# Optimization experiments

Hardware: AMD Instinct MI355X
Metric: run time of the kernel (lower is better)

## Reference

```python
import jax, jax.numpy as jnp
import numpy as np

N_NODES = 50000
N_EDGES = 800000
NFEAT = 512
NHID = 64
NHEADS = 8
NCLASS = 40
ALPHA = 0.2  # LeakyReLU slope
EPS = 1e-16  # guards isolated-node division


def setup_inputs() -> dict:
    key = jax.random.key(0)
    k = jax.random.split(key, 6)
    x = jax.random.normal(k[0], (N_NODES, NFEAT), dtype=jnp.float32)
    W_heads = jax.random.normal(k[1], (NHEADS, NFEAT, NHID), dtype=jnp.float32) * 0.05
    a_heads = jax.random.normal(k[2], (NHEADS, 2 * NHID), dtype=jnp.float32) * 0.05
    W_out = jax.random.normal(k[3], (NHEADS * NHID, NCLASS), dtype=jnp.float32) * 0.05
    a_out = jax.random.normal(k[4], (2 * NCLASS,), dtype=jnp.float32) * 0.05
    edge_index = jax.random.randint(k[5], (2, N_EDGES), 0, N_NODES, dtype=jnp.int32)
    return {"x": x, "W_heads": W_heads, "a_heads": a_heads,
            "W_out": W_out, "a_out": a_out, "edge_index": edge_index}


def _gat_layer(x, W, a, row, col, concat):
    # pyGAT sparse layer: h = xW; e_ij = exp(-LeakyReLU(a^T [h_i || h_j]));
    # out_i = sum_j e_ij h_j / sum_j e_ij   (aggregate into row, gather from col)
    D = W.shape[1]
    h = x @ W                                            # [N, D]
    score = h[row] @ a[:D] + h[col] @ a[D:]              # [E]
    e = jnp.exp(-jax.nn.leaky_relu(score, ALPHA))        # [E]
    num = jax.ops.segment_sum(e[:, None] * h[col], row, num_segments=x.shape[0])  # [N, D]
    den = jax.ops.segment_sum(e, row, num_segments=x.shape[0])                    # [N]
    out = num / (den[:, None] + EPS)
    return jax.nn.elu(out) if concat else out


def reference(x, W_heads, a_heads, W_out, a_out, edge_index):
    # dropout layers are identity in eval mode (training=False)
    row, col = edge_index[0], edge_index[1]
    heads = jax.vmap(lambda W, a: _gat_layer(x, W, a, row, col, True))(W_heads, a_heads)
    # [H, N, D] -> [N, H*D] (concat along feature dim, head-major like torch.cat)
    hcat = jnp.transpose(heads, (1, 0, 2)).reshape(x.shape[0], -1)
    return _gat_layer(hcat, W_out, a_out, row, col, False)  # [N, NCLASS]
```

## Files before the change

### kernel.cpp

```cpp
#include <hip/hip_runtime.h>
#include <hip/hip_bf16.h>

#define N_NODES 50000
#define N_EDGES 800000
#define NFEAT   512
#define NHID    64
#define NHEADS  8
#define NCLASS  40
#define HD      (NHEADS*NHID)
#define ALPHA   0.2f
#define EPS_F   1e-16f
#define NCHUNK  ((N_NODES + 255)/256)

typedef __attribute__((ext_vector_type(8))) short short8;
typedef __attribute__((ext_vector_type(4))) float floatx4;

__device__ __forceinline__ float bf2f(unsigned short u) {
    union { unsigned int i; float f; } v; v.i = ((unsigned int)u) << 16; return v.f;
}
__device__ __forceinline__ unsigned short f2bf(float f) {
    union { __hip_bfloat16 h; unsigned short u; } cv;
    cv.h = __float2bfloat16(f);
    return cv.u;
}

__global__ void castX(const float* __restrict__ x, unsigned short* __restrict__ xb) {
    int idx = blockIdx.x*256 + threadIdx.x;
    if (idx >= N_NODES*512/4) return;
    float4 v = ((const float4*)x)[idx];
    ushort4 o;
    o.x = f2bf(v.x); o.y = f2bf(v.y); o.z = f2bf(v.z); o.w = f2bf(v.w);
    ((ushort4*)xb)[idx] = o;
}

__global__ void repackWb(const float* __restrict__ Wh, unsigned short* __restrict__ Wrb) {
    int idx = blockIdx.x*256 + threadIdx.x;
    if (idx >= 512*512) return;
    int n = idx >> 9, k = idx & 511;
    int hd = n >> 6, d = n & 63;
    Wrb[idx] = f2bf(Wh[(size_t)hd*NFEAT*NHID + (size_t)k*NHID + d]);
}

__global__ void repackWout(const float* __restrict__ Wo, unsigned short* __restrict__ Wob) {
    int idx = blockIdx.x*256 + threadIdx.x;
    if (idx >= 64*512) return;
    int n = idx >> 9, k = idx & 511;
    float v = (n < NCLASS) ? Wo[(size_t)k*NCLASS + n] : 0.f;
    Wob[idx] = f2bf(v);
}

__global__ __launch_bounds__(256) void mfma_gemm(const unsigned short* __restrict__ Abf,
                                                 const unsigned short* __restrict__ Bbf,
                                                 unsigned short* __restrict__ H1b, int M) {
    __shared__ short Asl[128*40];
    __shared__ short Bsl[128*40];
    int tid  = threadIdx.x;
    int wid  = tid >> 6, lane = tid & 63;
    int lrow = lane & 15, quad = lane >> 4;
    int wm = wid & 1, wn = wid >> 1;
    int row0 = blockIdx.y * 128, col0 = blockIdx.x * 128;

    floatx4 acc[4][4];
#pragma unroll
    for (int mm = 0; mm < 4; mm++)
#pragma unroll
        for (int nn = 0; nn < 4; nn++) acc[mm][nn] = (floatx4){0.f,0.f,0.f,0.f};

    for (int k0 = 0; k0 < 512; k0 += 32) {
#pragma unroll
        for (int it = 0; it < 2; ++it) {
            int q  = tid + it*256;
            int r  = q >> 2, kk = (q & 3) * 8;
            int ar = row0 + r; ar = ar < M ? ar : M - 1;
            *(short8*)(&Asl[r*40 + kk]) =
                *(const short8*)(Abf + (size_t)ar*512 + k0 + kk);
            *(short8*)(&Bsl[r*40 + kk]) =
                *(const short8*)(Bbf + (size_t)(col0 + r)*512 + k0 + kk);
        }
        __syncthreads();
        short8 af[4], bfr[4];
#pragma unroll
        for (int mm = 0; mm < 4; ++mm)
            af[mm] = *(const short8*)(&Asl[(wm*64 + mm*16 + lrow)*40 + quad*8]);
#pragma unroll
        for (int nn = 0; nn < 4; ++nn)
            bfr[nn] = *(const short8*)(&Bsl[(wn*64 + nn*16 + lrow)*40 + quad*8]);
#pragma unroll
        for (int mm = 0; mm < 4; ++mm)
#pragma unroll
            for (int nn = 0; nn < 4; ++nn)
                acc[mm][nn] = __builtin_amdgcn_mfma_f32_16x16x32_bf16(
                    af[mm], bfr[nn], acc[mm][nn], 0, 0, 0);
        __syncthreads();
    }

#pragma unroll
    for (int mm = 0; mm < 4; ++mm) {
        int rbase = row0 + wm*64 + mm*16 + quad*4;
#pragma unroll
        for (int nn = 0; nn < 4; ++nn) {
            int c = col0 + wn*64 + nn*16 + lrow;
#pragma unroll
            for (int r = 0; r < 4; ++r) {
                int grow = rbase + r;
                if (grow < M)
                    H1b[(size_t)grow*512 + c] = f2bf(acc[mm][nn][r]);
            }
        }
    }
}

__global__ __launch_bounds__(256) void mfma_gemm2(const unsigned short* __restrict__ Abf,
                                                  const unsigned short* __restrict__ Bbf,
                                                  float* __restrict__ H2, int M) {
    __shared__ short Asl[256*40];
    __shared__ short Bsl[64*40];
    int tid  = threadIdx.x;
    int wid  = tid >> 6, lane = tid & 63;
    int lrow = lane & 15, quad = lane >> 4;
    int row0 = blockIdx.x * 256;

    floatx4 acc[4][4];
#pragma unroll
    for (int mm = 0; mm < 4; mm++)
#pragma unroll
        for (int nn = 0; nn < 4; nn++) acc[mm][nn] = (floatx4){0.f,0.f,0.f,0.f};

    for (int k0 = 0; k0 < 512; k0 += 32) {
#pragma unroll
        for (int it = 0; it < 4; ++it) {
            int q  = tid + it*256;
            int r  = q >> 2, kk = (q & 3) * 8;
            int ar = row0 + r; ar = ar < M ? ar : M - 1;
            *(short8*)(&Asl[r*40 + kk]) =
                *(const short8*)(Abf + (size_t)ar*512 + k0 + kk);
        }
        {
            int r = tid >> 2, kk = (tid & 3) * 8;
            *(short8*)(&Bsl[r*40 + kk]) =
                *(const short8*)(Bbf + (size_t)r*512 + k0 + kk);
        }
        __syncthreads();
        short8 af[4], bfr[4];
#pragma unroll
        for (int mm = 0; mm < 4; ++mm)
            af[mm] = *(const short8*)(&Asl[(wid*64 + mm*16 + lrow)*40 + quad*8]);
#pragma unroll
        for (int nn = 0; nn < 4; ++nn)
            bfr[nn] = *(const short8*)(&Bsl[(nn*16 + lrow)*40 + quad*8]);
#pragma unroll
        for (int mm = 0; mm < 4; ++mm)
#pragma unroll
            for (int nn = 0; nn < 4; ++nn)
                acc[mm][nn] = __builtin_amdgcn_mfma_f32_16x16x32_bf16(
                    af[mm], bfr[nn], acc[mm][nn], 0, 0, 0);
        __syncthreads();
    }

#pragma unroll
    for (int mm = 0; mm < 4; ++mm) {
        int rbase = row0 + wid*64 + mm*16 + quad*4;
#pragma unroll
        for (int nn = 0; nn < 4; ++nn) {
            int c = nn*16 + lrow;
            if (c < NCLASS) {
#pragma unroll
                for (int r = 0; r < 4; ++r) {
                    int grow = rbase + r;
                    if (grow < M)
                        H2[(size_t)grow*NCLASS + c] = acc[mm][nn][r];
                }
            }
        }
    }
}

__global__ void dots1(const unsigned short* __restrict__ H1b,
                      const float* __restrict__ a_heads,
                      float* __restrict__ srcdot, float* __restrict__ dstdot) {
    int t = blockIdx.x*256 + threadIdx.x;
    if (t >= N_NODES*NHEADS) return;
    int i = t >> 3, hd = t & 7;
    const unsigned short* hrow = H1b + (size_t)i*HD + hd*NHID;
    const float* as = a_heads + hd*2*NHID;
    const float* ad = as + NHID;
    float s0 = 0.f, s1 = 0.f;
#pragma unroll
    for (int d = 0; d < NHID; d += 8) {
        short8 hv = *(const short8*)(hrow + d);
#pragma unroll
        for (int j = 0; j < 8; j++) {
            float h = bf2f((unsigned short)hv[j]);
            s0 = fmaf(h, as[d+j], s0);
            s1 = fmaf(h, ad[d+j], s1);
        }
    }
    srcdot[t] = s0; dstdot[t] = s1;
}

__global__ void edge_w1(const int* __restrict__ row, const int* __restrict__ col,
                        const float* __restrict__ srcdot, const float* __restrict__ dstdot,
                        float* __restrict__ Wedge) {
    int e = blockIdx.x*256 + threadIdx.x;
    if (e >= N_EDGES) return;
    int r = row[e], c = col[e];
    float4 sa = *(const float4*)(srcdot + (size_t)r*8);
    float4 sb = *(const float4*)(srcdot + (size_t)r*8 + 4);
    float4 da = *(const float4*)(dstdot + (size_t)c*8);
    float4 db = *(const float4*)(dstdot + (size_t)c*8 + 4);
    float s[8] = {sa.x+da.x, sa.y+da.y, sa.z+da.z, sa.w+da.w,
                  sb.x+db.x, sb.y+db.y, sb.z+db.z, sb.w+db.w};
    float o[8];
#pragma unroll
    for (int j = 0; j < 8; j++) {
        float lr = s[j] > 0.f ? s[j] : ALPHA*s[j];
        o[j] = __expf(-lr);
    }
    *(float4*)(Wedge + (size_t)e*8)     = make_float4(o[0], o[1], o[2], o[3]);
    *(float4*)(Wedge + (size_t)e*8 + 4) = make_float4(o[4], o[5], o[6], o[7]);
}

__global__ void zero_deg(int* __restrict__ deg) {
    int i = blockIdx.x*256 + threadIdx.x;
    if (i < N_NODES) deg[i] = 0;
}
__global__ void histk(const int* __restrict__ row, int* __restrict__ deg) {
    int e = blockIdx.x*256 + threadIdx.x;
    if (e < N_EDGES) atomicAdd(&deg[row[e]], 1);
}
__global__ void scanA(const int* __restrict__ deg, int* __restrict__ row_ptr,
                      int* __restrict__ chunk_tot) {
    __shared__ int s[256];
    int t = threadIdx.x;
    int idx = blockIdx.x*256 + t;
    int v = (idx < N_NODES) ? deg[idx] : 0;
    s[t] = v;
    __syncthreads();
#pragma unroll
    for (int off = 1; off < 256; off <<= 1) {
        int x = (t >= off) ? s[t-off] : 0;
        __syncthreads();
        s[t] += x;
        __syncthreads();
    }
    if (idx < N_NODES) row_ptr[idx] = s[t] - v;
    if (t == 255) chunk_tot[blockIdx.x] = s[t];
}
__global__ void scanB(const int* __restrict__ chunk_tot, int* __restrict__ chunk_off,
                      int* __restrict__ row_ptr) {
    __shared__ int s[256];
    int t = threadIdx.x;
    int v = (t < NCHUNK) ? chunk_tot[t] : 0;
    s[t] = v;
    __syncthreads();
#pragma unroll
    for (int off = 1; off < 256; off <<= 1) {
        int x = (t >= off) ? s[t-off] : 0;
        __syncthreads();
        s[t] += x;
        __syncthreads();
    }
    if (t < NCHUNK) chunk_off[t] = s[t] - v;
    if (t == 255) row_ptr[N_NODES] = s[t];
}
__global__ void scanC(const int* __restrict__ chunk_off, int* __restrict__ row_ptr,
                      int* __restrict__ cursor) {
    int idx = blockIdx.x*256 + threadIdx.x;
    if (idx < N_NODES) {
        int rp = row_ptr[idx] + chunk_off[idx >> 8];
        row_ptr[idx] = rp;
        cursor[idx] = rp;
    }
}
__global__ void fillk(const int* __restrict__ row, const int* __restrict__ col,
                      int* __restrict__ cursor, int* __restrict__ csr_eid,
                      int* __restrict__ csr_col) {
    int e = blockIdx.x*256 + threadIdx.x;
    if (e >= N_EDGES) return;
    int r = row[e];
    int pos = atomicAdd(&cursor[r], 1);
    csr_eid[pos] = e;
    csr_col[pos] = col[e];
}

__global__ __launch_bounds__(256) void agg1(const unsigned short* __restrict__ H1b,
                                            const float* __restrict__ Wedge,
                                            const int* __restrict__ row_ptr,
                                            const int* __restrict__ csr_eid,
                                            const int* __restrict__ csr_col,
                                            unsigned short* __restrict__ hcatb) {
    int wave = (blockIdx.x*256 + threadIdx.x) >> 6;
    int lane = threadIdx.x & 63;
    if (wave >= N_NODES) return;
    int start = row_ptr[wave], end = row_ptr[wave+1];
    float acc[8], den[8];
#pragma unroll
    for (int j = 0; j < 8; j++) { acc[j] = 0.f; den[j] = 0.f; }

    int k = start;
    for (; k + 2 <= end; k += 2) {
        int e0 = csr_eid[k], e1 = csr_eid[k+1];
        int c0 = csr_col[k], c1 = csr_col[k+1];
        float4 wa0 = *(const float4*)(Wedge + (size_t)e0*8);
        float4 wb0 = *(const float4*)(Wedge + (size_t)e0*8 + 4);
        float4 wa1 = *(const float4*)(Wedge + (size_t)e1*8);
        float4 wb1 = *(const float4*)(Wedge + (size_t)e1*8 + 4);
        const unsigned short* r0 = H1b + (size_t)c0*HD + lane;
        const unsigned short* r1 = H1b + (size_t)c1*HD + lane;
        float h0[8], h1[8];
#pragma unroll
        for (int j = 0; j < 8; j++) { h0[j] = bf2f(r0[j*64]); h1[j] = bf2f(r1[j*64]); }
        float w0[8] = {wa0.x, wa0.y, wa0.z, wa0.w, wb0.x, wb0.y, wb0.z, wb0.w};
        float w1[8] = {wa1.x, wa1.y, wa1.z, wa1.w, wb1.x, wb1.y, wb1.z, wb1.w};
#pragma unroll
        for (int j = 0; j < 8; j++) {
            den[j] += w0[j] + w1[j];
            acc[j] = fmaf(w0[j], h0[j], acc[j]);
            acc[j] = fmaf(w1[j], h1[j], acc[j]);
        }
    }
    for (; k < end; ++k) {
        int e = csr_eid[k];
        int c = csr_col[k];
        float4 wa = *(const float4*)(Wedge + (size_t)e*8);
        float4 wb = *(const float4*)(Wedge + (size_t)e*8 + 4);
        const unsigned short* r0 = H1b + (size_t)c*HD + lane;
        float w[8] = {wa.x, wa.y, wa.z, wa.w, wb.x, wb.y, wb.z, wb.w};
#pragma unroll
        for (int j = 0; j < 8; j++) {
            float h = bf2f(r0[j*64]);
            den[j] += w[j];
            acc[j] = fmaf(w[j], h, acc[j]);
        }
    }
#pragma unroll
    for (int j = 0; j < 8; j++) {
        float o = acc[j] / (den[j] + EPS_F);
        o = o > 0.f ? o : (__expf(o) - 1.f);
        hcatb[(size_t)wave*HD + j*64 + lane] = f2bf(o);
    }
}

__global__ void dots2(const float* __restrict__ H2, const float* __restrict__ a_out,
                      float* __restrict__ src2, float* __restrict__ dst2) {
    int i = blockIdx.x*256 + threadIdx.x;
    if (i >= N_NODES) return;
    float s0 = 0.f, s1 = 0.f;
#pragma unroll
    for (int c = 0; c < NCLASS; c++) {
        float h = H2[(size_t)i*NCLASS + c];
        s0 = fmaf(h, a_out[c], s0);
        s1 = fmaf(h, a_out[NCLASS + c], s1);
    }
    src2[i] = s0; dst2[i] = s1;
}

__global__ void edge_w2(const int* __restrict__ row, const int* __restrict__ col,
                        const float* __restrict__ src2, const float* __restrict__ dst2,
                        float* __restrict__ w2) {
    int e = blockIdx.x*256 + threadIdx.x;
    if (e >= N_EDGES) return;
    float s = src2[row[e]] + dst2[col[e]];
    float lr = s > 0.f ? s : ALPHA*s;
    w2[e] = __expf(-lr);
}

__global__ __launch_bounds__(256) void agg2(const float* __restrict__ H2,
                                            const float* __restrict__ w2,
                                            const int* __restrict__ row_ptr,
                                            const int* __restrict__ csr_eid,
                                            const int* __restrict__ csr_col,
                                            float* __restrict__ out) {
    int wave = (blockIdx.x*256 + threadIdx.x) >> 6;
    int lane = threadIdx.x & 63;
    if (wave >= N_NODES) return;
    int start = row_ptr[wave], end = row_ptr[wave+1];
    int l = lane < NCLASS ? lane : 0;
    float acc = 0.f, den = 0.f;
    int k = start;
    for (; k + 4 <= end; k += 4) {
        int e0 = csr_eid[k],   e1 = csr_eid[k+1], e2 = csr_eid[k+2], e3 = csr_eid[k+3];
        int c0 = csr_col[k],   c1 = csr_col[k+1], c2 = csr_col[k+2], c3 = csr_col[k+3];
        float w0 = w2[e0], w1 = w2[e1], w2v = w2[e2], w3 = w2[e3];
        float h0 = H2[(size_t)c0*NCLASS + l];
        float h1 = H2[(size_t)c1*NCLASS + l];
        float h2 = H2[(size_t)c2*NCLASS + l];
        float h3 = H2[(size_t)c3*NCLASS + l];
        den += (w0 + w1) + (w2v + w3);
        acc = fmaf(w0, h0, acc);
        acc = fmaf(w1, h1, acc);
        acc = fmaf(w2v, h2, acc);
        acc = fmaf(w3, h3, acc);
    }
    for (; k < end; ++k) {
        int e = csr_eid[k];
        int c = csr_col[k];
        float w = w2[e];
        den += w;
        acc = fmaf(w, H2[(size_t)c*NCLASS + l], acc);
    }
    if (lane < NCLASS)
        out[(size_t)wave*NCLASS + lane] = acc / (den + EPS_F);
}

extern "C" void kernel_launch(void* const* d_in, const int* in_sizes, int n_in,
                              void* d_out, int out_size, void* d_ws, size_t ws_size,
                              hipStream_t stream) {
    const float* x       = (const float*)d_in[0];
    const float* W_heads = (const float*)d_in[1];
    const float* a_heads = (const float*)d_in[2];
    const float* W_out   = (const float*)d_in[3];
    const float* a_out   = (const float*)d_in[4];
    const int*   ei      = (const int*)d_in[5];
    const int*   row     = ei;
    const int*   col     = ei + N_EDGES;
    float* out = (float*)d_out;

    char* ws = (char*)d_ws;
    size_t off = 0;
    auto alloc = [&](size_t bytes) {
        char* p = ws + off;
        off = (off + bytes + 255) & ~(size_t)255;
        return p;
    };
    unsigned short* Wrb   = (unsigned short*)alloc((size_t)512*512*2);
    unsigned short* Wob   = (unsigned short*)alloc((size_t)64*512*2);
    unsigned short* xb    = (unsigned short*)alloc((size_t)N_NODES*512*2);
    unsigned short* H1b   = (unsigned short*)alloc((size_t)N_NODES*HD*2);
    unsigned short* hcatb = (unsigned short*)alloc((size_t)N_NODES*HD*2);
    float* srcdot  = (float*)alloc((size_t)N_NODES*NHEADS*4);
    float* dstdot  = (float*)alloc((size_t)N_NODES*NHEADS*4);
    float* Wedge   = (float*)alloc((size_t)N_EDGES*NHEADS*4);
    int*   deg     = (int*)alloc((size_t)N_NODES*4);
    int*   row_ptr = (int*)alloc((size_t)(N_NODES+1)*4);
    int*   cursor  = (int*)alloc((size_t)N_NODES*4);
    int*   ctot    = (int*)alloc(256*4);
    int*   coff    = (int*)alloc(256*4);
    int*   csr_eid = (int*)alloc((size_t)N_EDGES*4);
    int*   csr_col = (int*)alloc((size_t)N_EDGES*4);
    float* H2      = (float*)alloc((size_t)N_NODES*NCLASS*4);
    float* src2    = (float*)alloc((size_t)N_NODES*4);
    float* dst2    = (float*)alloc((size_t)N_NODES*4);
    float* w2      = (float*)alloc((size_t)N_EDGES*4);
    (void)ws_size;

    const int EB = (N_EDGES + 255)/256;
    const int NB = (N_NODES + 255)/256;

    castX<<<(N_NODES*512/4 + 255)/256, 256, 0, stream>>>(x, xb);
    repackWb<<<(512*512 + 255)/256, 256, 0, stream>>>(W_heads, Wrb);
    repackWout<<<(64*512 + 255)/256, 256, 0, stream>>>(W_out, Wob);
    {
        dim3 grid(4, (N_NODES + 127)/128);
        mfma_gemm<<<grid, 256, 0, stream>>>(xb, Wrb, H1b, N_NODES);
    }
    dots1<<<(N_NODES*NHEADS + 255)/256, 256, 0, stream>>>(H1b, a_heads, srcdot, dstdot);
    edge_w1<<<EB, 256, 0, stream>>>(row, col, srcdot, dstdot, Wedge);

    zero_deg<<<NB, 256, 0, stream>>>(deg);
    histk<<<EB, 256, 0, stream>>>(row, deg);
    scanA<<<NCHUNK, 256, 0, stream>>>(deg, row_ptr, ctot);
    scanB<<<1, 256, 0, stream>>>(ctot, coff, row_ptr);
    scanC<<<NCHUNK, 256, 0, stream>>>(coff, row_ptr, cursor);
    fillk<<<EB, 256, 0, stream>>>(row, col, cursor, csr_eid, csr_col);

    agg1<<<(N_NODES*64 + 255)/256, 256, 0, stream>>>(H1b, Wedge, row_ptr,
                                                     csr_eid, csr_col, hcatb);

    mfma_gemm2<<<(N_NODES + 255)/256, 256, 0, stream>>>(hcatb, Wob, H2, N_NODES);
    dots2<<<NB, 256, 0, stream>>>(H2, a_out, src2, dst2);
    edge_w2<<<EB, 256, 0, stream>>>(row, col, src2, dst2, w2);
    agg2<<<(N_NODES*64 + 255)/256, 256, 0, stream>>>(H2, w2, row_ptr,
                                                     csr_eid, csr_col, out);
}
```

Measured before the change: 568.0 us.

## Fuse x cast into GEMM, interleave H1 layout, store edge weights in CSR order

The fp32-to-bf16 cast of x moves into the first GEMM's shared-memory load, so the separate cast kernel and its intermediate buffer go away. GEMM1 writes H1 in a head-interleaved layout, letting each lane load all 8 heads of one feature as a single 16-byte vector in both dots1 and agg1. Edge-weight computation is fused into the CSR fill kernel and written at the CSR position, and layer-2 weights are scattered through a saved position array. This removes the csr_eid indirection and gives contiguous weight reads in the aggregation kernels. The cost is scattered writes and a per-element conversion inside the GEMM load loop.

```diff
diff --git a/kernel.cpp b/kernel.cpp
--- a/kernel.cpp
+++ b/kernel.cpp
@@ -24,15 +24,6 @@
     return cv.u;
 }
 
-__global__ void castX(const float* __restrict__ x, unsigned short* __restrict__ xb) {
-    int idx = blockIdx.x*256 + threadIdx.x;
-    if (idx >= N_NODES*512/4) return;
-    float4 v = ((const float4*)x)[idx];
-    ushort4 o;
-    o.x = f2bf(v.x); o.y = f2bf(v.y); o.z = f2bf(v.z); o.w = f2bf(v.w);
-    ((ushort4*)xb)[idx] = o;
-}
-
 __global__ void repackWb(const float* __restrict__ Wh, unsigned short* __restrict__ Wrb) {
     int idx = blockIdx.x*256 + threadIdx.x;
     if (idx >= 512*512) return;
@@ -49,9 +40,9 @@
     Wob[idx] = f2bf(v);
 }
 
-__global__ __launch_bounds__(256) void mfma_gemm(const unsigned short* __restrict__ Abf,
-                                                 const unsigned short* __restrict__ Bbf,
-                                                 unsigned short* __restrict__ H1b, int M) {
+__global__ __launch_bounds__(256) void mfma_gemm1(const float* __restrict__ A,
+                                                  const unsigned short* __restrict__ Bbf,
+                                                  unsigned short* __restrict__ H1p, int M) {
     __shared__ short Asl[128*40];
     __shared__ short Bsl[128*40];
     int tid  = threadIdx.x;
@@ -72,8 +63,15 @@
             int q  = tid + it*256;
             int r  = q >> 2, kk = (q & 3) * 8;
             int ar = row0 + r; ar = ar < M ? ar : M - 1;
-            *(short8*)(&Asl[r*40 + kk]) =
-                *(const short8*)(Abf + (size_t)ar*512 + k0 + kk);
+            const float* src = A + (size_t)ar*512 + k0 + kk;
+            float4 f0 = *(const float4*)src;
+            float4 f1 = *(const float4*)(src + 4);
+            short8 h;
+            h[0] = (short)f2bf(f0.x); h[1] = (short)f2bf(f0.y);
+            h[2] = (short)f2bf(f0.z); h[3] = (short)f2bf(f0.w);
+            h[4] = (short)f2bf(f1.x); h[5] = (short)f2bf(f1.y);
+            h[6] = (short)f2bf(f1.z); h[7] = (short)f2bf(f1.w);
+            *(short8*)(&Asl[r*40 + kk]) = h;
             *(short8*)(&Bsl[r*40 + kk]) =
                 *(const short8*)(Bbf + (size_t)(col0 + r)*512 + k0 + kk);
         }
@@ -100,11 +98,12 @@
 #pragma unroll
         for (int nn = 0; nn < 4; ++nn) {
             int c = col0 + wn*64 + nn*16 + lrow;
+            int off = (c & 63)*8 + (c >> 6);
 #pragma unroll
             for (int r = 0; r < 4; ++r) {
                 int grow = rbase + r;
                 if (grow < M)
-                    H1b[(size_t)grow*512 + c] = f2bf(acc[mm][nn][r]);
+                    H1p[(size_t)grow*512 + off] = f2bf(acc[mm][nn][r]);
             }
         }
     }
@@ -175,49 +174,36 @@
     }
 }
 
-__global__ void dots1(const unsigned short* __restrict__ H1b,
-                      const float* __restrict__ a_heads,
-                      float* __restrict__ srcdot, float* __restrict__ dstdot) {
-    int t = blockIdx.x*256 + threadIdx.x;
-    if (t >= N_NODES*NHEADS) return;
-    int i = t >> 3, hd = t & 7;
-    const unsigned short* hrow = H1b + (size_t)i*HD + hd*NHID;
-    const float* as = a_heads + hd*2*NHID;
-    const float* ad = as + NHID;
-    float s0 = 0.f, s1 = 0.f;
-#pragma unroll
-    for (int d = 0; d < NHID; d += 8) {
-        short8 hv = *(const short8*)(hrow + d);
+__global__ __launch_bounds__(256) void dots1(const unsigned short* __restrict__ H1p,
+                                             const float* __restrict__ a_heads,
+                                             float* __restrict__ srcdot,
+                                             float* __restrict__ dstdot) {
+    int wave = (blockIdx.x*256 + threadIdx.x) >> 6;
+    int lane = threadIdx.x & 63;
+    if (wave >= N_NODES) return;
+    short8 hv = *(const short8*)(H1p + (size_t)wave*512 + lane*8);
+    float s0[8], s1[8];
+#pragma unroll
+    for (int j = 0; j < 8; j++) {
+        float h = bf2f((unsigned short)hv[j]);
+        s0[j] = h * a_heads[j*128 + lane];
+        s1[j] = h * a_heads[j*128 + 64 + lane];
+    }
+#pragma unroll
+    for (int off = 32; off > 0; off >>= 1) {
 #pragma unroll
         for (int j = 0; j < 8; j++) {
-            float h = bf2f((unsigned short)hv[j]);
-            s0 = fmaf(h, as[d+j], s0);
-            s1 = fmaf(h, ad[d+j], s1);
-        }
-    }
-    srcdot[t] = s0; dstdot[t] = s1;
-}
-
-__global__ void edge_w1(const int* __restrict__ row, const int* __restrict__ col,
-                        const float* __restrict__ srcdot, const float* __restrict__ dstdot,
-                        float* __restrict__ Wedge) {
-    int e = blockIdx.x*256 + threadIdx.x;
-    if (e >= N_EDGES) return;
-    int r = row[e], c = col[e];
-    float4 sa = *(const float4*)(srcdot + (size_t)r*8);
-    float4 sb = *(const float4*)(srcdot + (size_t)r*8 + 4);
-    float4 da = *(const float4*)(dstdot + (size_t)c*8);
-    float4 db = *(const float4*)(dstdot + (size_t)c*8 + 4);
-    float s[8] = {sa.x+da.x, sa.y+da.y, sa.z+da.z, sa.w+da.w,
-                  sb.x+db.x, sb.y+db.y, sb.z+db.z, sb.w+db.w};
-    float o[8];
-#pragma unroll
-    for (int j = 0; j < 8; j++) {
-        float lr = s[j] > 0.f ? s[j] : ALPHA*s[j];
-        o[j] = __expf(-lr);
-    }
-    *(float4*)(Wedge + (size_t)e*8)     = make_float4(o[0], o[1], o[2], o[3]);
-    *(float4*)(Wedge + (size_t)e*8 + 4) = make_float4(o[4], o[5], o[6], o[7]);
+            s0[j] += __shfl_down(s0[j], off, 64);
+            s1[j] += __shfl_down(s1[j], off, 64);
+        }
+    }
+    if (lane == 0) {
+#pragma unroll
+        for (int j = 0; j < 8; j++) {
+            srcdot[wave*8 + j] = s0[j];
+            dstdot[wave*8 + j] = s1[j];
+        }
+    }
 }
 
 __global__ void zero_deg(int* __restrict__ deg) {
@@ -272,21 +258,36 @@
         cursor[idx] = rp;
     }
 }
-__global__ void fillk(const int* __restrict__ row, const int* __restrict__ col,
-                      int* __restrict__ cursor, int* __restrict__ csr_eid,
-                      int* __restrict__ csr_col) {
+
+__global__ void fillk_w1(const int* __restrict__ row, const int* __restrict__ col,
+                         const float* __restrict__ srcdot, const float* __restrict__ dstdot,
+                         int* __restrict__ cursor, int* __restrict__ csr_col,
+                         int* __restrict__ pose, float* __restrict__ Wcsr) {
     int e = blockIdx.x*256 + threadIdx.x;
     if (e >= N_EDGES) return;
-    int r = row[e];
+    int r = row[e], c = col[e];
     int pos = atomicAdd(&cursor[r], 1);
-    csr_eid[pos] = e;
-    csr_col[pos] = col[e];
-}
-
-__global__ __launch_bounds__(256) void agg1(const unsigned short* __restrict__ H1b,
-                                            const float* __restrict__ Wedge,
+    csr_col[pos] = c;
+    pose[e] = pos;
+    float4 sa = *(const float4*)(srcdot + (size_t)r*8);
+    float4 sb = *(const float4*)(srcdot + (size_t)r*8 + 4);
+    float4 da = *(const float4*)(dstdot + (size_t)c*8);
+    float4 db = *(const float4*)(dstdot + (size_t)c*8 + 4);
+    float s[8] = {sa.x+da.x, sa.y+da.y, sa.z+da.z, sa.w+da.w,
+                  sb.x+db.x, sb.y+db.y, sb.z+db.z, sb.w+db.w};
+    float o[8];
+#pragma unroll
+    for (int j = 0; j < 8; j++) {
+        float lr = s[j] > 0.f ? s[j] : ALPHA*s[j];
+        o[j] = __expf(-lr);
+    }
+    *(float4*)(Wcsr + (size_t)pos*8)     = make_float4(o[0], o[1], o[2], o[3]);
+    *(float4*)(Wcsr + (size_t)pos*8 + 4) = make_float4(o[4], o[5], o[6], o[7]);
+}
+
+__global__ __launch_bounds__(256) void agg1(const unsigned short* __restrict__ H1p,
+                                            const float* __restrict__ Wcsr,
                                             const int* __restrict__ row_ptr,
-                                            const int* __restrict__ csr_eid,
                                             const int* __restrict__ csr_col,
                                             unsigned short* __restrict__ hcatb) {
     int wave = (blockIdx.x*256 + threadIdx.x) >> 6;
@@ -299,38 +300,32 @@
 
     int k = start;
     for (; k + 2 <= end; k += 2) {
-        int e0 = csr_eid[k], e1 = csr_eid[k+1];
         int c0 = csr_col[k], c1 = csr_col[k+1];
-        float4 wa0 = *(const float4*)(Wedge + (size_t)e0*8);
-        float4 wb0 = *(const float4*)(Wedge + (size_t)e0*8 + 4);
-        float4 wa1 = *(const float4*)(Wedge + (size_t)e1*8);
-        float4 wb1 = *(const float4*)(Wedge + (size_t)e1*8 + 4);
-        const unsigned short* r0 = H1b + (size_t)c0*HD + lane;
-        const unsigned short* r1 = H1b + (size_t)c1*HD + lane;
-        float h0[8], h1[8];
-#pragma unroll
-        for (int j = 0; j < 8; j++) { h0[j] = bf2f(r0[j*64]); h1[j] = bf2f(r1[j*64]); }
+        float4 wa0 = *(const float4*)(Wcsr + (size_t)k*8);
+        float4 wb0 = *(const float4*)(Wcsr + (size_t)k*8 + 4);
+        float4 wa1 = *(const float4*)(Wcsr + (size_t)k*8 + 8);
+        float4 wb1 = *(const float4*)(Wcsr + (size_t)k*8 + 12);
+        short8 hv0 = *(const short8*)(H1p + (size_t)c0*512 + lane*8);
+        short8 hv1 = *(const short8*)(H1p + (size_t)c1*512 + lane*8);
         float w0[8] = {wa0.x, wa0.y, wa0.z, wa0.w, wb0.x, wb0.y, wb0.z, wb0.w};
         float w1[8] = {wa1.x, wa1.y, wa1.z, wa1.w, wb1.x, wb1.y, wb1.z, wb1.w};
 #pragma unroll
         for (int j = 0; j < 8; j++) {
             den[j] += w0[j] + w1[j];
-            acc[j] = fmaf(w0[j], h0[j], acc[j]);
-            acc[j] = fmaf(w1[j], h1[j], acc[j]);
+            acc[j] = fmaf(w0[j], bf2f((unsigned short)hv0[j]), acc[j]);
+            acc[j] = fmaf(w1[j], bf2f((unsigned short)hv1[j]), acc[j]);
         }
     }
     for (; k < end; ++k) {
-        int e = csr_eid[k];
         int c = csr_col[k];
-        float4 wa = *(const float4*)(Wedge + (size_t)e*8);
-        float4 wb = *(const float4*)(Wedge + (size_t)e*8 + 4);
-        const unsigned short* r0 = H1b + (size_t)c*HD + lane;
+        float4 wa = *(const float4*)(Wcsr + (size_t)k*8);
+        float4 wb = *(const float4*)(Wcsr + (size_t)k*8 + 4);
+        short8 hv = *(const short8*)(H1p + (size_t)c*512 + lane*8);
         float w[8] = {wa.x, wa.y, wa.z, wa.w, wb.x, wb.y, wb.z, wb.w};
 #pragma unroll
         for (int j = 0; j < 8; j++) {
-            float h = bf2f(r0[j*64]);
             den[j] += w[j];
-            acc[j] = fmaf(w[j], h, acc[j]);
+            acc[j] = fmaf(w[j], bf2f((unsigned short)hv[j]), acc[j]);
         }
     }
 #pragma unroll
@@ -356,19 +351,19 @@
 }
 
 __global__ void edge_w2(const int* __restrict__ row, const int* __restrict__ col,
+                        const int* __restrict__ pose,
                         const float* __restrict__ src2, const float* __restrict__ dst2,
-                        float* __restrict__ w2) {
+                        float* __restrict__ w2csr) {
     int e = blockIdx.x*256 + threadIdx.x;
     if (e >= N_EDGES) return;
     float s = src2[row[e]] + dst2[col[e]];
     float lr = s > 0.f ? s : ALPHA*s;
-    w2[e] = __expf(-lr);
+    w2csr[pose[e]] = __expf(-lr);
 }
 
 __global__ __launch_bounds__(256) void agg2(const float* __restrict__ H2,
-                                            const float* __restrict__ w2,
+                                            const float* __restrict__ w2csr,
                                             const int* __restrict__ row_ptr,
-                                            const int* __restrict__ csr_eid,
                                             const int* __restrict__ csr_col,
                                             float* __restrict__ out) {
     int wave = (blockIdx.x*256 + threadIdx.x) >> 6;
@@ -379,23 +374,21 @@
     float acc = 0.f, den = 0.f;
     int k = start;
     for (; k + 4 <= end; k += 4) {
-        int e0 = csr_eid[k],   e1 = csr_eid[k+1], e2 = csr_eid[k+2], e3 = csr_eid[k+3];
+        float4 wv = *(const float4*)(w2csr + k);
         int c0 = csr_col[k],   c1 = csr_col[k+1], c2 = csr_col[k+2], c3 = csr_col[k+3];
-        float w0 = w2[e0], w1 = w2[e1], w2v = w2[e2], w3 = w2[e3];
         float h0 = H2[(size_t)c0*NCLASS + l];
         float h1 = H2[(size_t)c1*NCLASS + l];
         float h2 = H2[(size_t)c2*NCLASS + l];
         float h3 = H2[(size_t)c3*NCLASS + l];
-        den += (w0 + w1) + (w2v + w3);
-        acc = fmaf(w0, h0, acc);
-        acc = fmaf(w1, h1, acc);
-        acc = fmaf(w2v, h2, acc);
-        acc = fmaf(w3, h3, acc);
+        den += (wv.x + wv.y) + (wv.z + wv.w);
+        acc = fmaf(wv.x, h0, acc);
+        acc = fmaf(wv.y, h1, acc);
+        acc = fmaf(wv.z, h2, acc);
+        acc = fmaf(wv.w, h3, acc);
     }
     for (; k < end; ++k) {
-        int e = csr_eid[k];
         int c = csr_col[k];
-        float w = w2[e];
+        float w = w2csr[k];
         den += w;
         acc = fmaf(w, H2[(size_t)c*NCLASS + l], acc);
     }
@@ -425,51 +418,48 @@
     };
     unsigned short* Wrb   = (unsigned short*)alloc((size_t)512*512*2);
     unsigned short* Wob   = (unsigned short*)alloc((size_t)64*512*2);
-    unsigned short* xb    = (unsigned short*)alloc((size_t)N_NODES*512*2);
-    unsigned short* H1b   = (unsigned short*)alloc((size_t)N_NODES*HD*2);
+    unsigned short* H1p   = (unsigned short*)alloc((size_t)N_NODES*HD*2);
     unsigned short* hcatb = (unsigned short*)alloc((size_t)N_NODES*HD*2);
     float* srcdot  = (float*)alloc((size_t)N_NODES*NHEADS*4);
     float* dstdot  = (float*)alloc((size_t)N_NODES*NHEADS*4);
-    float* Wedge   = (float*)alloc((size_t)N_EDGES*NHEADS*4);
+    float* Wcsr    = (float*)alloc((size_t)N_EDGES*NHEADS*4);
     int*   deg     = (int*)alloc((size_t)N_NODES*4);
     int*   row_ptr = (int*)alloc((size_t)(N_NODES+1)*4);
     int*   cursor  = (int*)alloc((size_t)N_NODES*4);
     int*   ctot    = (int*)alloc(256*4);
     int*   coff    = (int*)alloc(256*4);
-    int*   csr_eid = (int*)alloc((size_t)N_EDGES*4);
     int*   csr_col = (int*)alloc((size_t)N_EDGES*4);
+    int*   pose    = (int*)alloc((size_t)N_EDGES*4);
     float* H2      = (float*)alloc((size_t)N_NODES*NCLASS*4);
     float* src2    = (float*)alloc((size_t)N_NODES*4);
     float* dst2    = (float*)alloc((size_t)N_NODES*4);
-    float* w2      = (float*)alloc((size_t)N_EDGES*4);
+    float* w2csr   = (float*)alloc((size_t)N_EDGES*4);
     (void)ws_size;
 
     const int EB = (N_EDGES + 255)/256;
     const int NB = (N_NODES + 255)/256;
-
-    castX<<<(N_NODES*512/4 + 255)/256, 256, 0, stream>>>(x, xb);
+    const int WB = (N_NODES*64 + 255)/256;
+
     repackWb<<<(512*512 + 255)/256, 256, 0, stream>>>(W_heads, Wrb);
     repackWout<<<(64*512 + 255)/256, 256, 0, stream>>>(W_out, Wob);
     {
         dim3 grid(4, (N_NODES + 127)/128);
-        mfma_gemm<<<grid, 256, 0, stream>>>(xb, Wrb, H1b, N_NODES);
-    }
-    dots1<<<(N_NODES*NHEADS + 255)/256, 256, 0, stream>>>(H1b, a_heads, srcdot, dstdot);
-    edge_w1<<<EB, 256, 0, stream>>>(row, col, srcdot, dstdot, Wedge);
+        mfma_gemm1<<<grid, 256, 0, stream>>>(x, Wrb, H1p, N_NODES);
+    }
+    dots1<<<WB, 256, 0, stream>>>(H1p, a_heads, srcdot, dstdot);
 
     zero_deg<<<NB, 256, 0, stream>>>(deg);
     histk<<<EB, 256, 0, stream>>>(row, deg);
     scanA<<<NCHUNK, 256, 0, stream>>>(deg, row_ptr, ctot);
     scanB<<<1, 256, 0, stream>>>(ctot, coff, row_ptr);
     scanC<<<NCHUNK, 256, 0, stream>>>(coff, row_ptr, cursor);
-    fillk<<<EB, 256, 0, stream>>>(row, col, cursor, csr_eid, csr_col);
-
-    agg1<<<(N_NODES*64 + 255)/256, 256, 0, stream>>>(H1b, Wedge, row_ptr,
-                                                     csr_eid, csr_col, hcatb);
+    fillk_w1<<<EB, 256, 0, stream>>>(row, col, srcdot, dstdot, cursor,
+                                     csr_col, pose, Wcsr);
+
+    agg1<<<WB, 256, 0, stream>>>(H1p, Wcsr, row_ptr, csr_col, hcatb);
 
     mfma_gemm2<<<(N_NODES + 255)/256, 256, 0, stream>>>(hcatb, Wob, H2, N_NODES);
     dots2<<<NB, 256, 0, stream>>>(H2, a_out, src2, dst2);
-    edge_w2<<<EB, 256, 0, stream>>>(row, col, src2, dst2, w2);
-    agg2<<<(N_NODES*64 + 255)/256, 256, 0, stream>>>(H2, w2, row_ptr,
-                                                     csr_eid, csr_col, out);
-}
+    edge_w2<<<EB, 256, 0, stream>>>(row, col, pose, src2, dst2, w2csr);
+    agg2<<<WB, 256, 0, stream>>>(H2, w2csr, row_ptr, csr_col, out);
+}
```

Measured after the change: 578.7 us. Within noise of the previous version (+1.9%).
